# Performance work log

Hardware: AMD Instinct MI355X
Metric: run time of the kernel (lower is better)

The kernel has to match this reference:

```python
import jax, jax.numpy as jnp
import numpy as np

D_MODEL = 64
N_HEAD = 8
MAX_REL = 16  # module hardcodes max_relative_position = 16
B, S = 8, 1024


def _linear_params(k, fan_in, fan_out):
    kw, kb = jax.random.split(k)
    s = 1.0 / np.sqrt(fan_in)
    W = jax.random.uniform(kw, (fan_in, fan_out), jnp.float32, -s, s)
    b = jax.random.uniform(kb, (fan_out,), jnp.float32, -s, s)
    return W, b


def setup_inputs() -> dict:
    key = jax.random.key(0)
    ks = jax.random.split(key, 10)
    Wq, bq = _linear_params(ks[0], D_MODEL, D_MODEL * N_HEAD)
    Wk, bk = _linear_params(ks[1], D_MODEL, D_MODEL * N_HEAD)
    Wv, bv = _linear_params(ks[2], D_MODEL, D_MODEL * N_HEAD)
    Wo, bo = _linear_params(ks[3], D_MODEL * N_HEAD, D_MODEL)
    Wkr, bkr = _linear_params(ks[4], D_MODEL, D_MODEL)
    Wqr, bqr = _linear_params(ks[5], D_MODEL, D_MODEL)
    p = jax.random.normal(ks[6], (2 * MAX_REL + 1, D_MODEL), jnp.float32)
    query = jax.random.normal(ks[7], (B, S, D_MODEL), jnp.float32)
    key_t = jax.random.normal(ks[8], (B, S, D_MODEL), jnp.float32)
    value = jax.random.normal(ks[9], (B, S, D_MODEL), jnp.float32)
    return dict(query=query, key=key_t, value=value,
                Wq=Wq, bq=bq, Wk=Wk, bk=bk, Wv=Wv, bv=bv,
                Wo=Wo, bo=bo, Wkr=Wkr, bkr=bkr, Wqr=Wqr, bqr=bqr, p=p)


def reference(query, key, value, Wq, bq, Wk, bk, Wv, bv, Wo, bo, Wkr, bkr, Wqr, bqr, p):
    Bsz, Sq, d = query.shape
    H = Wq.shape[1] // d  # head_dim == d_model in this module
    scale = jnp.sqrt(jnp.asarray(3 * d, jnp.float32))

    def heads(x, W, b):
        return (x @ W + b).reshape(Bsz, -1, H, d).transpose(0, 2, 1, 3)  # [B,H,S,d]

    q1 = heads(query, Wq, bq)
    k1 = heads(key, Wk, bk)
    v1 = heads(value, Wv, bv)

    # content-content term
    attn1 = jnp.einsum('bhqd,bhkd->bhqk', q1, k1)

    # relative-position terms. make_table uses clamp(dist, min=16, max=16)+16,
    # so every gather index is exactly 2*MAX_REL -> the gathered value is the
    # single column 2*MAX_REL of each table, broadcast over the last axis.
    k_r = p @ Wkr + bkr  # [2*MAX_REL+1, d]
    q_r = p @ Wqr + bqr
    attn2 = jnp.einsum('bhqd,d->bhq', q1, k_r[2 * MAX_REL])[..., None]  # [B,H,Sq,1]
    attn3 = jnp.einsum('bhkd,d->bhk', k1, q_r[2 * MAX_REL])[..., None]  # [B,H,Sk,1] (Sk==Sq)

    attn = jax.nn.softmax((attn1 + attn2 + attn3) / scale, axis=-1)
    x = jnp.einsum('bhqk,bhkd->bhqd', attn, v1)
    x = x.transpose(0, 2, 1, 3).reshape(Bsz, Sq, H * d)
    return x @ Wo + bo
```

## Files before the change

kernel.cpp:

```cpp
#include <hip/hip_runtime.h>
#include <hip/hip_bf16.h>


#define N_HEAD 8
#define BATCH  8
#define SEQ    1024
#define DMH    512
#define SC2    0.10411804386480816f

typedef __hip_bfloat16 bf16;
typedef __bf16 bf16x8 __attribute__((ext_vector_type(8)));
typedef float  f32x4  __attribute__((ext_vector_type(4)));

__global__ __launch_bounds__(256)
void init_kernel(const float* __restrict__ Wo, const float* __restrict__ bo,
                 float* __restrict__ out, bf16* __restrict__ WoT)
{
    const int idx = blockIdx.x * 256 + threadIdx.x;
    out[idx] = bo[idx & 63];
    if (idx < 512 * 64) {
        const int k = idx >> 6, c = idx & 63;
        WoT[(size_t)c * 512 + k] = __float2bfloat16(Wo[idx]);
    }
}

__global__ __launch_bounds__(256)
void qkv_proj_kernel(const float* __restrict__ Xq, const float* __restrict__ Xk,
                     const float* __restrict__ Xv,
                     const float* __restrict__ Wq, const float* __restrict__ bq,
                     const float* __restrict__ Wk, const float* __restrict__ bk,
                     const float* __restrict__ Wv, const float* __restrict__ bv,
                     bf16* __restrict__ Qh, bf16* __restrict__ Kh,
                     bf16* __restrict__ Vt)
{
    const int rt    = blockIdx.x;
    const int ct    = blockIdx.y;
    const int which = blockIdx.z;

    const float* __restrict__ X    = which == 0 ? Xq : (which == 1 ? Xk : Xv);
    const float* __restrict__ W    = which == 0 ? Wq : (which == 1 ? Wk : Wv);
    const float* __restrict__ bias = which == 0 ? bq : (which == 1 ? bk : bv);

    __shared__ float Xs[64][65];
    __shared__ float Ws[64][68];

    const int tid = threadIdx.x;
    for (int i = tid; i < 1024; i += 256) {
        const int r = i >> 4, c4 = (i & 15) << 2;
        const float4 xv = *(const float4*)&X[(size_t)(rt * 64 + r) * 64 + c4];
        Xs[r][c4 + 0] = xv.x; Xs[r][c4 + 1] = xv.y;
        Xs[r][c4 + 2] = xv.z; Xs[r][c4 + 3] = xv.w;
        *(float4*)&Ws[r][c4] = *(const float4*)&W[(size_t)r * DMH + ct * 64 + c4];
    }
    __syncthreads();

    const int r  = tid & 63;
    const int cg = tid >> 6;

    float acc[16];
#pragma unroll
    for (int j = 0; j < 16; j++) acc[j] = 0.f;

#pragma unroll 4
    for (int kk = 0; kk < 64; kk++) {
        const float x = Xs[r][kk];
#pragma unroll
        for (int j4 = 0; j4 < 4; j4++) {
            const float4 w = *(const float4*)&Ws[kk][cg * 16 + j4 * 4];
            acc[j4 * 4 + 0] += x * w.x;
            acc[j4 * 4 + 1] += x * w.y;
            acc[j4 * 4 + 2] += x * w.z;
            acc[j4 * 4 + 3] += x * w.w;
        }
    }

    const int row = rt * 64 + r;
    const int b   = row >> 10;
    const int s   = row & 1023;
    if (which == 2) {
        bf16* dstT = Vt + (((size_t)b * N_HEAD + ct) * 64 + cg * 16) * SEQ + s;
#pragma unroll
        for (int j = 0; j < 16; j++)
            dstT[(size_t)j * SEQ] = __float2bfloat16(acc[j] + bias[ct * 64 + cg * 16 + j]);
    } else {
        const float sc = (which == 0) ? SC2 : 1.0f;
        bf16* O   = which == 0 ? Qh : Kh;
        bf16* dst = O + (((size_t)b * N_HEAD + ct) * SEQ + s) * 64 + cg * 16;
#pragma unroll
        for (int j = 0; j < 16; j++)
            dst[j] = __float2bfloat16((acc[j] + bias[ct * 64 + cg * 16 + j]) * sc);
    }
}

__global__ __launch_bounds__(512, 4)
void flash_attn_kernel(const bf16* __restrict__ Qh, const bf16* __restrict__ Kh,
                       const bf16* __restrict__ Vt, const bf16* __restrict__ WoT,
                       float* __restrict__ out)
{
    const int qt   = blockIdx.x;
    const int h    = blockIdx.y;
    const int b    = blockIdx.z;
    const int tid  = threadIdx.x;
    const int wave = tid >> 6;
    const int w4   = wave & 3;
    const int kh   = wave >> 2;
    const int lane = tid & 63;
    const int t16  = lane & 15;
    const int quad = lane >> 4;

    const size_t bh = (size_t)b * N_HEAD + h;
    const bf16* __restrict__ Qp  = Qh + bh * (SEQ * 64);
    const bf16* __restrict__ Kp  = Kh + bh * (SEQ * 64);
    const bf16* __restrict__ Vtp = Vt + bh * (64 * SEQ);

    __shared__ __align__(16) bf16 smem[36864];
    bf16* KsB  = smem;
    bf16* VtsB = smem + 9216;
    bf16* PsB  = smem + 18432;

    bf16x8 qf0[2], qf1[2];
#pragma unroll
    for (int rs = 0; rs < 2; rs++) {
        const int qrow = qt * 128 + rs * 64 + w4 * 16 + t16;
        qf0[rs] = *(const bf16x8*)(Qp + (size_t)qrow * 64 + 0  + quad * 8);
        qf1[rs] = *(const bf16x8*)(Qp + (size_t)qrow * 64 + 32 + quad * 8);
    }

    f32x4 Of[2][4];
    float l_i[2][4];
#pragma unroll
    for (int rs = 0; rs < 2; rs++) {
#pragma unroll
        for (int nt = 0; nt < 4; nt++) Of[rs][nt] = (f32x4){0.f, 0.f, 0.f, 0.f};
#pragma unroll
        for (int rr = 0; rr < 4; rr++) l_i[rs][rr] = 0.f;
    }

    for (int kt = 0; kt < 8; kt++) {
#pragma unroll
        for (int i = tid; i < 2048; i += 512) {
            const int khs = i >> 10;
            const int j   = i & 1023;
            const int vk  = j >> 9;
            const int r8  = (j & 511) >> 3;
            const int c8  = (j & 7) << 3;
            if (vk == 0)
                *(bf16x8*)&KsB[khs * 4608 + r8 * 72 + c8] =
                    *(const bf16x8*)&Kp[(size_t)(khs * 512 + kt * 64 + r8) * 64 + c8];
            else
                *(bf16x8*)&VtsB[khs * 4608 + r8 * 72 + c8] =
                    *(const bf16x8*)&Vtp[(size_t)r8 * SEQ + khs * 512 + kt * 64 + c8];
        }
        __syncthreads();

        const bf16* Ksw  = KsB  + kh * 4608;
        const bf16* Vtsw = VtsB + kh * 4608;

#pragma unroll
        for (int rs = 0; rs < 2; rs++) {
            f32x4 Sf[4];
#pragma unroll
            for (int nt = 0; nt < 4; nt++) {
                Sf[nt] = (f32x4){0.f, 0.f, 0.f, 0.f};
                const bf16x8 kf0 = *(const bf16x8*)&Ksw[(nt * 16 + t16) * 72 + 0  + quad * 8];
                const bf16x8 kf1 = *(const bf16x8*)&Ksw[(nt * 16 + t16) * 72 + 32 + quad * 8];
                Sf[nt] = __builtin_amdgcn_mfma_f32_16x16x32_bf16(qf0[rs], kf0, Sf[nt], 0, 0, 0);
                Sf[nt] = __builtin_amdgcn_mfma_f32_16x16x32_bf16(qf1[rs], kf1, Sf[nt], 0, 0, 0);
            }

#pragma unroll
            for (int nt = 0; nt < 4; nt++)
#pragma unroll
                for (int rr = 0; rr < 4; rr++) {
                    const float p = exp2f(Sf[nt][rr]);
                    Sf[nt][rr] = p;
                    l_i[rs][rr] += p;
                }

            bf16* Psw = PsB + (rs * 8 + wave) * 1152;
#pragma unroll
            for (int nt = 0; nt < 4; nt++)
#pragma unroll
                for (int rr = 0; rr < 4; rr++)
                    Psw[(quad * 4 + rr) * 72 + nt * 16 + t16] =
                        __float2bfloat16(Sf[nt][rr]);

            const bf16x8 pf0 = *(const bf16x8*)&Psw[t16 * 72 + 0  + quad * 8];
            const bf16x8 pf1 = *(const bf16x8*)&Psw[t16 * 72 + 32 + quad * 8];
#pragma unroll
            for (int nt = 0; nt < 4; nt++) {
                const bf16x8 vf0 = *(const bf16x8*)&Vtsw[(nt * 16 + t16) * 72 + 0  + quad * 8];
                const bf16x8 vf1 = *(const bf16x8*)&Vtsw[(nt * 16 + t16) * 72 + 32 + quad * 8];
                Of[rs][nt] = __builtin_amdgcn_mfma_f32_16x16x32_bf16(pf0, vf0, Of[rs][nt], 0, 0, 0);
                Of[rs][nt] = __builtin_amdgcn_mfma_f32_16x16x32_bf16(pf1, vf1, Of[rs][nt], 0, 0, 0);
            }
        }
        __syncthreads();
    }

    float* Xch = (float*)smem;
    float* Lch = (float*)(smem + 16384);
    bf16*  WoS = smem + 20480;
    bf16*  Pe  = smem + 25088;

    if (kh == 1) {
#pragma unroll
        for (int rs = 0; rs < 2; rs++) {
#pragma unroll
            for (int nt = 0; nt < 4; nt++)
#pragma unroll
                for (int rr = 0; rr < 4; rr++)
                    Xch[((w4 * 2 + rs) * 64 + lane) * 16 + nt * 4 + rr] = Of[rs][nt][rr];
#pragma unroll
            for (int rr = 0; rr < 4; rr++)
                Lch[((w4 * 2 + rs) * 64 + lane) * 4 + rr] = l_i[rs][rr];
        }
    }
    {
        const int r8 = tid >> 3, c8 = (tid & 7) << 3;
        *(bf16x8*)&WoS[r8 * 72 + c8] = *(const bf16x8*)&WoT[(size_t)r8 * 512 + h * 64 + c8];
    }
    __syncthreads();

    if (kh == 0) {
#pragma unroll
        for (int rs = 0; rs < 2; rs++) {
#pragma unroll
            for (int nt = 0; nt < 4; nt++)
#pragma unroll
                for (int rr = 0; rr < 4; rr++)
                    Of[rs][nt][rr] += Xch[((w4 * 2 + rs) * 64 + lane) * 16 + nt * 4 + rr];
#pragma unroll
            for (int rr = 0; rr < 4; rr++)
                l_i[rs][rr] += Lch[((w4 * 2 + rs) * 64 + lane) * 4 + rr];
        }

#pragma unroll
        for (int rs = 0; rs < 2; rs++)
#pragma unroll
            for (int off = 8; off >= 1; off >>= 1)
#pragma unroll
                for (int rr = 0; rr < 4; rr++)
                    l_i[rs][rr] += __shfl_xor(l_i[rs][rr], off, 64);

        bf16* Pew = Pe + w4 * 1152;
#pragma unroll
        for (int rs = 0; rs < 2; rs++) {
            float inv_l[4];
#pragma unroll
            for (int rr = 0; rr < 4; rr++) inv_l[rr] = 1.0f / l_i[rs][rr];
#pragma unroll
            for (int nt = 0; nt < 4; nt++)
#pragma unroll
                for (int rr = 0; rr < 4; rr++)
                    Pew[(quad * 4 + rr) * 72 + nt * 16 + t16] =
                        __float2bfloat16(Of[rs][nt][rr] * inv_l[rr]);

            const bf16x8 pf0 = *(const bf16x8*)&Pew[t16 * 72 + 0  + quad * 8];
            const bf16x8 pf1 = *(const bf16x8*)&Pew[t16 * 72 + 32 + quad * 8];

            f32x4 R[4];
#pragma unroll
            for (int nt = 0; nt < 4; nt++) {
                R[nt] = (f32x4){0.f, 0.f, 0.f, 0.f};
                const bf16x8 wf0 = *(const bf16x8*)&WoS[(nt * 16 + t16) * 72 + 0  + quad * 8];
                const bf16x8 wf1 = *(const bf16x8*)&WoS[(nt * 16 + t16) * 72 + 32 + quad * 8];
                R[nt] = __builtin_amdgcn_mfma_f32_16x16x32_bf16(pf0, wf0, R[nt], 0, 0, 0);
                R[nt] = __builtin_amdgcn_mfma_f32_16x16x32_bf16(pf1, wf1, R[nt], 0, 0, 0);
            }

            const int srow_base = qt * 128 + rs * 64 + w4 * 16 + quad * 4;
#pragma unroll
            for (int rr = 0; rr < 4; rr++) {
                const size_t base = ((size_t)b * SEQ + srow_base + rr) * 64;
#pragma unroll
                for (int nt = 0; nt < 4; nt++)
                    atomicAdd(&out[base + nt * 16 + t16], R[nt][rr]);
            }
        }
    }
}

extern "C" void kernel_launch(void* const* d_in, const int* in_sizes, int n_in,
                              void* d_out, int out_size, void* d_ws, size_t ws_size,
                              hipStream_t stream)
{
    const float* query = (const float*)d_in[0];
    const float* key_  = (const float*)d_in[1];
    const float* value = (const float*)d_in[2];
    const float* Wq    = (const float*)d_in[3];
    const float* bq    = (const float*)d_in[4];
    const float* Wk    = (const float*)d_in[5];
    const float* bk    = (const float*)d_in[6];
    const float* Wv    = (const float*)d_in[7];
    const float* bv    = (const float*)d_in[8];
    const float* Wo    = (const float*)d_in[9];
    const float* bo    = (const float*)d_in[10];

    float* out = (float*)d_out;
    char* ws   = (char*)d_ws;
    bf16* Qh  = (bf16*)(ws + (size_t) 0 * 1024 * 1024);
    bf16* Kh  = (bf16*)(ws + (size_t) 8 * 1024 * 1024);
    bf16* Vt  = (bf16*)(ws + (size_t)16 * 1024 * 1024);
    bf16* WoT = (bf16*)(ws + (size_t)24 * 1024 * 1024);

    init_kernel<<<dim3(2048), 256, 0, stream>>>(Wo, bo, out, WoT);
    qkv_proj_kernel<<<dim3(128, 8, 3), 256, 0, stream>>>(
        query, key_, value, Wq, bq, Wk, bk, Wv, bv, Qh, Kh, Vt);
    flash_attn_kernel<<<dim3(8, 8, 8), 512, 0, stream>>>(Qh, Kh, Vt, WoT, out);
}
```

Measured before the change: 164.8 us.

## Use bf16 MFMA for QKV projection with pre-transposed bf16 weights

Replaces the scalar fp32 FMA QKV projection with a 16x16x32 bf16 MFMA kernel that processes 128-row tiles. The init kernel now also converts and transposes Wq/Wk/Wv to bf16. The V output is staged through shared memory so the transposed Vt writes become coalesced 16-byte stores. Inputs are rounded to bf16 before the matmul, which adds precision loss, and the new path relies on the extra weight-conversion work in the init kernel.

```diff
diff --git a/kernel.cpp b/kernel.cpp
--- a/kernel.cpp
+++ b/kernel.cpp
@@ -10,26 +10,39 @@
 
 typedef __hip_bfloat16 bf16;
 typedef __bf16 bf16x8 __attribute__((ext_vector_type(8)));
+typedef __bf16 bf16x4 __attribute__((ext_vector_type(4)));
 typedef float  f32x4  __attribute__((ext_vector_type(4)));
 
 __global__ __launch_bounds__(256)
-void init_kernel(const float* __restrict__ Wo, const float* __restrict__ bo,
-                 float* __restrict__ out, bf16* __restrict__ WoT)
+void init_kernel(const float* __restrict__ Wq, const float* __restrict__ Wk,
+                 const float* __restrict__ Wv, const float* __restrict__ Wo,
+                 const float* __restrict__ bo, float* __restrict__ out,
+                 bf16* __restrict__ WqT, bf16* __restrict__ WkT,
+                 bf16* __restrict__ WvT, bf16* __restrict__ WoT)
 {
     const int idx = blockIdx.x * 256 + threadIdx.x;
     out[idx] = bo[idx & 63];
     if (idx < 512 * 64) {
-        const int k = idx >> 6, c = idx & 63;
-        WoT[(size_t)c * 512 + k] = __float2bfloat16(Wo[idx]);
+        {
+            const int n = idx >> 6, k = idx & 63;
+            WqT[idx] = __float2bfloat16(Wq[(size_t)k * 512 + n]);
+            WkT[idx] = __float2bfloat16(Wk[(size_t)k * 512 + n]);
+            WvT[idx] = __float2bfloat16(Wv[(size_t)k * 512 + n]);
+        }
+        {
+            const int c = idx >> 9, k = idx & 511;
+            WoT[idx] = __float2bfloat16(Wo[(size_t)k * 64 + c]);
+        }
     }
 }
 
 __global__ __launch_bounds__(256)
-void qkv_proj_kernel(const float* __restrict__ Xq, const float* __restrict__ Xk,
+void qkv_mfma_kernel(const float* __restrict__ Xq, const float* __restrict__ Xk,
                      const float* __restrict__ Xv,
-                     const float* __restrict__ Wq, const float* __restrict__ bq,
-                     const float* __restrict__ Wk, const float* __restrict__ bk,
-                     const float* __restrict__ Wv, const float* __restrict__ bv,
+                     const bf16* __restrict__ WqT, const bf16* __restrict__ WkT,
+                     const bf16* __restrict__ WvT,
+                     const float* __restrict__ bq, const float* __restrict__ bk,
+                     const float* __restrict__ bv,
                      bf16* __restrict__ Qh, bf16* __restrict__ Kh,
                      bf16* __restrict__ Vt)
 {
@@ -37,58 +50,90 @@
     const int ct    = blockIdx.y;
     const int which = blockIdx.z;
 
-    const float* __restrict__ X    = which == 0 ? Xq : (which == 1 ? Xk : Xv);
-    const float* __restrict__ W    = which == 0 ? Wq : (which == 1 ? Wk : Wv);
-    const float* __restrict__ bias = which == 0 ? bq : (which == 1 ? bk : bv);
-
-    __shared__ float Xs[64][65];
-    __shared__ float Ws[64][68];
-
-    const int tid = threadIdx.x;
-    for (int i = tid; i < 1024; i += 256) {
+    const float* __restrict__ X    = which == 0 ? Xq  : (which == 1 ? Xk  : Xv);
+    const bf16*  __restrict__ WT   = which == 0 ? WqT : (which == 1 ? WkT : WvT);
+    const float* __restrict__ bias = which == 0 ? bq  : (which == 1 ? bk  : bv);
+
+    __shared__ __align__(16) bf16 Xs [128 * 72];
+    __shared__ __align__(16) bf16 Wts[64 * 72];
+    __shared__ float Bs[64];
+
+    const int tid  = threadIdx.x;
+    const int w4   = tid >> 6;
+    const int lane = tid & 63;
+    const int t16  = lane & 15;
+    const int quad = lane >> 4;
+
+    if (tid < 64) Bs[tid] = bias[ct * 64 + tid];
+    for (int i = tid; i < 2048; i += 256) {
         const int r = i >> 4, c4 = (i & 15) << 2;
-        const float4 xv = *(const float4*)&X[(size_t)(rt * 64 + r) * 64 + c4];
-        Xs[r][c4 + 0] = xv.x; Xs[r][c4 + 1] = xv.y;
-        Xs[r][c4 + 2] = xv.z; Xs[r][c4 + 3] = xv.w;
-        *(float4*)&Ws[r][c4] = *(const float4*)&W[(size_t)r * DMH + ct * 64 + c4];
+        const float4 v = *(const float4*)&X[(size_t)(rt * 128 + r) * 64 + c4];
+        bf16 t[4] = {__float2bfloat16(v.x), __float2bfloat16(v.y),
+                     __float2bfloat16(v.z), __float2bfloat16(v.w)};
+        *(bf16x4*)&Xs[r * 72 + c4] = *(bf16x4*)t;
+    }
+    for (int i = tid; i < 512; i += 256) {
+        const int r8 = i >> 3, c8 = (i & 7) << 3;
+        *(bf16x8*)&Wts[r8 * 72 + c8] = *(const bf16x8*)&WT[(size_t)(ct * 64 + r8) * 64 + c8];
     }
     __syncthreads();
 
-    const int r  = tid & 63;
-    const int cg = tid >> 6;
-
-    float acc[16];
-#pragma unroll
-    for (int j = 0; j < 16; j++) acc[j] = 0.f;
-
-#pragma unroll 4
-    for (int kk = 0; kk < 64; kk++) {
-        const float x = Xs[r][kk];
-#pragma unroll
-        for (int j4 = 0; j4 < 4; j4++) {
-            const float4 w = *(const float4*)&Ws[kk][cg * 16 + j4 * 4];
-            acc[j4 * 4 + 0] += x * w.x;
-            acc[j4 * 4 + 1] += x * w.y;
-            acc[j4 * 4 + 2] += x * w.z;
-            acc[j4 * 4 + 3] += x * w.w;
-        }
-    }
-
-    const int row = rt * 64 + r;
-    const int b   = row >> 10;
-    const int s   = row & 1023;
-    if (which == 2) {
-        bf16* dstT = Vt + (((size_t)b * N_HEAD + ct) * 64 + cg * 16) * SEQ + s;
-#pragma unroll
-        for (int j = 0; j < 16; j++)
-            dstT[(size_t)j * SEQ] = __float2bfloat16(acc[j] + bias[ct * 64 + cg * 16 + j]);
+    bf16x8 bf0[4], bf1[4];
+#pragma unroll
+    for (int nt = 0; nt < 4; nt++) {
+        bf0[nt] = *(const bf16x8*)&Wts[(nt * 16 + t16) * 72 + 0  + quad * 8];
+        bf1[nt] = *(const bf16x8*)&Wts[(nt * 16 + t16) * 72 + 32 + quad * 8];
+    }
+
+    f32x4 acc[2][4];
+#pragma unroll
+    for (int rs = 0; rs < 2; rs++) {
+        const int m = rs * 64 + w4 * 16 + t16;
+        const bf16x8 af0 = *(const bf16x8*)&Xs[m * 72 + 0  + quad * 8];
+        const bf16x8 af1 = *(const bf16x8*)&Xs[m * 72 + 32 + quad * 8];
+#pragma unroll
+        for (int nt = 0; nt < 4; nt++) {
+            acc[rs][nt] = (f32x4){0.f, 0.f, 0.f, 0.f};
+            acc[rs][nt] = __builtin_amdgcn_mfma_f32_16x16x32_bf16(af0, bf0[nt], acc[rs][nt], 0, 0, 0);
+            acc[rs][nt] = __builtin_amdgcn_mfma_f32_16x16x32_bf16(af1, bf1[nt], acc[rs][nt], 0, 0, 0);
+        }
+    }
+
+    const int b     = rt >> 3;
+    const int sbase = (rt & 7) * 128;
+
+    if (which < 2) {
+        bf16* O = which == 0 ? Qh : Kh;
+        const float sc = (which == 0) ? SC2 : 1.0f;
+#pragma unroll
+        for (int rs = 0; rs < 2; rs++)
+#pragma unroll
+            for (int rr = 0; rr < 4; rr++) {
+                const int s = sbase + rs * 64 + w4 * 16 + quad * 4 + rr;
+                bf16* dst = O + (((size_t)b * N_HEAD + ct) * SEQ + s) * 64 + t16;
+#pragma unroll
+                for (int nt = 0; nt < 4; nt++)
+                    dst[nt * 16] = __float2bfloat16((acc[rs][nt][rr] + Bs[nt * 16 + t16]) * sc);
+            }
     } else {
-        const float sc = (which == 0) ? SC2 : 1.0f;
-        bf16* O   = which == 0 ? Qh : Kh;
-        bf16* dst = O + (((size_t)b * N_HEAD + ct) * SEQ + s) * 64 + cg * 16;
-#pragma unroll
-        for (int j = 0; j < 16; j++)
-            dst[j] = __float2bfloat16((acc[j] + bias[ct * 64 + cg * 16 + j]) * sc);
+        __syncthreads();
+        bf16* VtS = Xs;
+#pragma unroll
+        for (int rs = 0; rs < 2; rs++)
+#pragma unroll
+            for (int nt = 0; nt < 4; nt++)
+#pragma unroll
+                for (int rr = 0; rr < 4; rr++) {
+                    const int rloc = rs * 64 + w4 * 16 + quad * 4 + rr;
+                    VtS[(nt * 16 + t16) * 136 + rloc] =
+                        __float2bfloat16(acc[rs][nt][rr] + Bs[nt * 16 + t16]);
+                }
+        __syncthreads();
+        for (int i = tid; i < 1024; i += 256) {
+            const int c = i >> 4, r8 = (i & 15) << 3;
+            *(bf16x8*)&Vt[(((size_t)b * N_HEAD + ct) * 64 + c) * SEQ + sbase + r8] =
+                *(const bf16x8*)&VtS[c * 136 + r8];
+        }
     }
 }
 
@@ -303,9 +348,13 @@
     bf16* Kh  = (bf16*)(ws + (size_t) 8 * 1024 * 1024);
     bf16* Vt  = (bf16*)(ws + (size_t)16 * 1024 * 1024);
     bf16* WoT = (bf16*)(ws + (size_t)24 * 1024 * 1024);
-
-    init_kernel<<<dim3(2048), 256, 0, stream>>>(Wo, bo, out, WoT);
-    qkv_proj_kernel<<<dim3(128, 8, 3), 256, 0, stream>>>(
-        query, key_, value, Wq, bq, Wk, bk, Wv, bv, Qh, Kh, Vt);
+    bf16* WqT = (bf16*)(ws + (size_t)24 * 1024 * 1024 + 65536);
+    bf16* WkT = (bf16*)(ws + (size_t)24 * 1024 * 1024 + 131072);
+    bf16* WvT = (bf16*)(ws + (size_t)24 * 1024 * 1024 + 196608);
+
+    init_kernel<<<dim3(2048), 256, 0, stream>>>(Wq, Wk, Wv, Wo, bo, out,
+                                                WqT, WkT, WvT, WoT);
+    qkv_mfma_kernel<<<dim3(64, 8, 3), 256, 0, stream>>>(
+        query, key_, value, WqT, WkT, WvT, bq, bk, bv, Qh, Kh, Vt);
     flash_attn_kernel<<<dim3(8, 8, 8), 512, 0, stream>>>(Qh, Kh, Vt, WoT, out);
 }
```

Measured after the change: 147.7 us. 1.12x faster.
